# Kernel tuning notes

Measured on AMD Instinct MI355X. Metric: run time of the kernel, lower is better.

The kernel has to match this reference:

```python
import jax, jax.numpy as jnp
import numpy as np

X = 32; Y = 32
H1 = (X + Y) * 10 * 8          # 5120
H2 = X * Y * 4                 # 4096
HID = 1 * (X * X + Y * Y)      # gru_scale_s=1 -> 2048
IN1 = 2 * X + Y + X * Y        # 1120
IN2 = 2 * Y + Y + X * Y        # 1120
OUT1 = X * X; OUT2 = Y * Y


def gru_cell(x, h, Wih, Whh, bih, bhh):
    # PyTorch GRU cell, gate order r,z,n
    gi = Wih @ x + bih
    gh = Whh @ h + bhh
    ir, iz, inn = jnp.split(gi, 3)
    hr, hz, hn = jnp.split(gh, 3)
    r = jax.nn.sigmoid(ir + hr)
    z = jax.nn.sigmoid(iz + hz)
    n = jnp.tanh(inn + r * hn)
    return (1.0 - z) * n + z * h


def setup_inputs() -> dict:
    key = jax.random.key(0)
    ks = iter(jax.random.split(key, 40))
    f32 = jnp.float32
    def rn(shape, scale=0.02):
        return (jax.random.normal(next(ks), shape, dtype=f32) * scale)
    inp = {
        'state_inno': rn((X, 1), 1.0),
        'observation_inno': rn((Y, 1), 1.0),
        'diff_state': rn((X, 1), 1.0),
        'diff_obs': rn((Y, 1), 1.0),
        'linearization_error': rn((Y, 1), 1.0),
        'Jacobian': rn((X * Y, 1), 1.0),
        'l1_W': rn((H1, IN1)), 'l1_b': rn((H1,)),
        'gru1_Wih': rn((3 * HID, H1)), 'gru1_Whh': rn((3 * HID, HID)),
        'gru1_bih': rn((3 * HID,)), 'gru1_bhh': rn((3 * HID,)),
        'l2_W1': rn((H2, HID)), 'l2_b1': rn((H2,)),
        'l2_W2': rn((OUT1, H2)), 'l2_b2': rn((OUT1,)),
        'l3_W': rn((H1, IN2)), 'l3_b': rn((H1,)),
        'gru2_Wih': rn((3 * HID, H1)), 'gru2_Whh': rn((3 * HID, HID)),
        'gru2_bih': rn((3 * HID,)), 'gru2_bhh': rn((3 * HID,)),
        'l4_W1': rn((H2, HID)), 'l4_b1': rn((H2,)),
        'l4_W2': rn((OUT2, H2)), 'l4_b2': rn((OUT2,)),
        'hn1': rn((HID,), 1.0),
        'hn2': rn((HID,), 1.0),
    }
    return inp


def reference(state_inno, observation_inno, diff_state, diff_obs,
              linearization_error, Jacobian,
              l1_W, l1_b, gru1_Wih, gru1_Whh, gru1_bih, gru1_bhh,
              l2_W1, l2_b1, l2_W2, l2_b2,
              l3_W, l3_b, gru2_Wih, gru2_Whh, gru2_bih, gru2_bhh,
              l4_W1, l4_b1, l4_W2, l4_b2, hn1, hn2):
    input1 = jnp.concatenate([state_inno, diff_state, linearization_error, Jacobian], axis=0).reshape(-1)
    input2 = jnp.concatenate([observation_inno, diff_obs, linearization_error, Jacobian], axis=0).reshape(-1)

    l1_out = jax.nn.relu(l1_W @ input1 + l1_b)           # [H1]
    h1 = gru_cell(l1_out, hn1, gru1_Wih, gru1_Whh, gru1_bih, gru1_bhh)  # [HID]
    l2_out = l2_W2 @ jax.nn.relu(l2_W1 @ h1 + l2_b1) + l2_b2
    Pk = l2_out.reshape(X, X)

    l3_out = jax.nn.relu(l3_W @ input2 + l3_b)
    h2 = gru_cell(l3_out, hn2, gru2_Wih, gru2_Whh, gru2_bih, gru2_bhh)
    l4_out = l4_W2 @ jax.nn.relu(l4_W1 @ h2 + l4_b1) + l4_b2
    Sk = l4_out.reshape(Y, Y)
    return (Pk, Sk)
```

## Files before the change

### kernel.cpp

```cpp
#include <hip/hip_runtime.h>
#include <hip/hip_bf16.h>

typedef __attribute__((ext_vector_type(4))) float f32x4;

#define TPB 256

#define IN1F   0
#define IN2F   1120
#define HN1F   2240
#define HN2F   4288
#define L1OUT  6336
#define L3OUT  11456
#define GH1    16576
#define GH2    22720
#define GI1    28864
#define GI2    35008
#define H1OFF  41152
#define H2OFF  43200
#define T1OFF  45248
#define T2OFF  49344


__device__ __forceinline__ void burst2(const float* a,
                                       f32x4& w0, f32x4& w1)
{
    asm volatile(
        "global_load_dwordx4 %0, %2, off\n\t"
        "global_load_dwordx4 %1, %2, off offset:1024\n\t"
        "s_waitcnt vmcnt(0)"
        : "=&v"(w0), "=&v"(w1)
        : "v"(a) : "memory");
}

__device__ __forceinline__ void burst4(const float* a,
                                       f32x4& w0, f32x4& w1, f32x4& w2, f32x4& w3)
{
    asm volatile(
        "global_load_dwordx4 %0, %4, off\n\t"
        "global_load_dwordx4 %1, %4, off offset:1024\n\t"
        "global_load_dwordx4 %2, %4, off offset:2048\n\t"
        "global_load_dwordx4 %3, %4, off offset:3072\n\t"
        "s_waitcnt vmcnt(0)"
        : "=&v"(w0), "=&v"(w1), "=&v"(w2), "=&v"(w3)
        : "v"(a) : "memory");
}

__device__ __forceinline__ void burst5_nt(const float* a, const float* a4,
                                          f32x4& w0, f32x4& w1, f32x4& w2,
                                          f32x4& w3, f32x4& w4)
{
    asm volatile(
        "global_load_dwordx4 %0, %5, off nt\n\t"
        "global_load_dwordx4 %1, %5, off offset:1024 nt\n\t"
        "global_load_dwordx4 %2, %5, off offset:2048 nt\n\t"
        "global_load_dwordx4 %3, %5, off offset:3072 nt\n\t"
        "global_load_dwordx4 %4, %6, off nt\n\t"
        "s_waitcnt vmcnt(0)"
        : "=&v"(w0), "=&v"(w1), "=&v"(w2), "=&v"(w3), "=&v"(w4)
        : "v"(a), "v"(a4) : "memory");
}

__device__ __forceinline__ float dot4(const f32x4& w, const f32x4& x) {
    return w[0]*x[0] + w[1]*x[1] + w[2]*x[2] + w[3]*x[3];
}

__device__ __forceinline__ float wave_reduce(float acc) {
#pragma unroll
    for (int off = 32; off; off >>= 1) acc += __shfl_xor(acc, off, 64);
    return acc;
}

__device__ __forceinline__ void stage_x(const float* __restrict__ x, float* xl, int K)
{
    for (int i = threadIdx.x; i < (K >> 2); i += TPB)
        ((f32x4*)xl)[i] = ((const f32x4*)x)[i];
    __syncthreads();
}


template <int ROWS>
__device__ __forceinline__ void mv5120(
    const float* __restrict__ W, const float* __restrict__ bias,
    float* xl, float* red, int row0, float* __restrict__ y, int act)
{
    const int wid  = threadIdx.x >> 6;
    const int lane = threadIdx.x & 63;
    const int c0   = lane * 4;
    const float* xw = xl + wid * 1280 + c0;

#pragma unroll
    for (int r = 0; r < ROWS; ++r) {
        const float* seg = W + (size_t)(row0 + r) * 5120 + wid * 1280 + c0;
        f32x4 w0, w1, w2, w3, w4;
        burst5_nt(seg, seg + 1024, w0, w1, w2, w3, w4);
        float acc = dot4(w0, *reinterpret_cast<const f32x4*>(xw))
                  + dot4(w1, *reinterpret_cast<const f32x4*>(xw + 256))
                  + dot4(w2, *reinterpret_cast<const f32x4*>(xw + 512))
                  + dot4(w3, *reinterpret_cast<const f32x4*>(xw + 768))
                  + dot4(w4, *reinterpret_cast<const f32x4*>(xw + 1024));
        acc = wave_reduce(acc);
        if (lane == 0) red[r * 4 + wid] = acc;
        __syncthreads();
    }
    if (threadIdx.x < ROWS) {
        int t = threadIdx.x;
        float v = red[t*4] + red[t*4+1] + red[t*4+2] + red[t*4+3] + bias[row0 + t];
        if (act) v = fmaxf(v, 0.f);
        y[row0 + t] = v;
    }
}

template <int ROWS>
__device__ __forceinline__ void mv2048(
    const float* __restrict__ W, const float* __restrict__ bias,
    float* xl, float* red, int row0, float* __restrict__ y, int act)
{
    const int wid  = threadIdx.x >> 6;
    const int lane = threadIdx.x & 63;
    const int c0   = lane * 4;
    const float* xw = xl + wid * 512 + c0;

#pragma unroll
    for (int r = 0; r < ROWS; ++r) {
        const float* seg = W + (size_t)(row0 + r) * 2048 + wid * 512 + c0;
        f32x4 w0, w1;
        burst2(seg, w0, w1);
        float acc = dot4(w0, *reinterpret_cast<const f32x4*>(xw))
                  + dot4(w1, *reinterpret_cast<const f32x4*>(xw + 256));
        acc = wave_reduce(acc);
        if (lane == 0) red[r * 4 + wid] = acc;
        __syncthreads();
    }
    if (threadIdx.x < ROWS) {
        int t = threadIdx.x;
        float v = red[t*4] + red[t*4+1] + red[t*4+2] + red[t*4+3] + bias[row0 + t];
        if (act) v = fmaxf(v, 0.f);
        y[row0 + t] = v;
    }
}

template <int ROWS>
__device__ __forceinline__ void mv4096(
    const float* __restrict__ W, const float* __restrict__ bias,
    float* xl, float* red, int row0, float* __restrict__ y, int act)
{
    const int wid  = threadIdx.x >> 6;
    const int lane = threadIdx.x & 63;
    const int c0   = lane * 4;
    const float* xw = xl + wid * 1024 + c0;

#pragma unroll
    for (int r = 0; r < ROWS; ++r) {
        const float* seg = W + (size_t)(row0 + r) * 4096 + wid * 1024 + c0;
        f32x4 w0, w1, w2, w3;
        burst4(seg, w0, w1, w2, w3);
        float acc = dot4(w0, *reinterpret_cast<const f32x4*>(xw))
                  + dot4(w1, *reinterpret_cast<const f32x4*>(xw + 256))
                  + dot4(w2, *reinterpret_cast<const f32x4*>(xw + 512))
                  + dot4(w3, *reinterpret_cast<const f32x4*>(xw + 768));
        acc = wave_reduce(acc);
        if (lane == 0) red[r * 4 + wid] = acc;
        __syncthreads();
    }
    if (threadIdx.x < ROWS) {
        int t = threadIdx.x;
        float v = red[t*4] + red[t*4+1] + red[t*4+2] + red[t*4+3] + bias[row0 + t];
        if (act) v = fmaxf(v, 0.f);
        y[row0 + t] = v;
    }
}

__device__ __forceinline__ void mv1120(
    const float* __restrict__ W, const float* __restrict__ bias,
    float* xl, int row0, float* __restrict__ y, int act)
{
    const int wid  = threadIdx.x >> 6;
    const int lane = threadIdx.x & 63;
    const int c0   = lane * 4;

#pragma unroll
    for (int step = 0; step < 2; ++step) {
        const int rr = row0 + step * 4 + wid;
        const float* Wr = W + (size_t)rr * 1120;
        f32x4 w0, w1, w2, w3;
        burst4(Wr + c0, w0, w1, w2, w3);
        float acc = dot4(w0, *reinterpret_cast<const f32x4*>(xl + c0))
                  + dot4(w1, *reinterpret_cast<const f32x4*>(xl + 256 + c0))
                  + dot4(w2, *reinterpret_cast<const f32x4*>(xl + 512 + c0))
                  + dot4(w3, *reinterpret_cast<const f32x4*>(xl + 768 + c0));
        if (c0 < 96) {
            const f32x4 wt = *reinterpret_cast<const f32x4*>(Wr + 1024 + c0);
            const f32x4 xt = *reinterpret_cast<const f32x4*>(xl + 1024 + c0);
            acc += dot4(wt, xt);
        }
        acc = wave_reduce(acc);
        if (lane == 0) {
            float v = acc + bias[rr];
            if (act) v = fmaxf(v, 0.f);
            y[rr] = v;
        }
    }
}

__global__ void k_prep(const float* __restrict__ state_inno,
                       const float* __restrict__ obs_inno,
                       const float* __restrict__ diff_state,
                       const float* __restrict__ diff_obs,
                       const float* __restrict__ lin_err,
                       const float* __restrict__ jac,
                       const float* __restrict__ hn1,
                       const float* __restrict__ hn2,
                       float* __restrict__ ws)
{
    int i = blockIdx.x * blockDim.x + threadIdx.x;
    if (i < 1120) {
        float v;
        if (i < 32)       v = state_inno[i];
        else if (i < 64)  v = diff_state[i - 32];
        else if (i < 96)  v = lin_err[i - 64];
        else              v = jac[i - 96];
        ws[IN1F + i] = v;
        float v2;
        if (i < 32)       v2 = obs_inno[i];
        else if (i < 64)  v2 = diff_obs[i - 32];
        else              v2 = v;
        ws[IN2F + i] = v2;
    }
    if (i < 2048) {
        ws[HN1F + i] = hn1[i];
        ws[HN2F + i] = hn2[i];
    }
}

__global__ void __launch_bounds__(TPB)
k_stageA(const float* l1_W, const float* l1_b,
         const float* l3_W, const float* l3_b,
         const float* Whh1, const float* bhh1,
         const float* Whh2, const float* bhh2,
         float* ws)
{
    __shared__ float xl[2048];
    __shared__ float red[8 * 4];
    int bid = blockIdx.x;
    if (bid < 640) {
        stage_x(ws + IN1F, xl, 1120);
        mv1120(l1_W, l1_b, xl, bid * 8, ws + L1OUT, 1);
    } else if (bid < 1280) {
        stage_x(ws + IN2F, xl, 1120);
        mv1120(l3_W, l3_b, xl, (bid - 640) * 8, ws + L3OUT, 1);
    } else if (bid < 2048) {
        stage_x(ws + HN1F, xl, 2048);
        mv2048<8>(Whh1, bhh1, xl, red, (bid - 1280) * 8, ws + GH1, 0);
    } else {
        stage_x(ws + HN2F, xl, 2048);
        mv2048<8>(Whh2, bhh2, xl, red, (bid - 2048) * 8, ws + GH2, 0);
    }
}

__global__ void __launch_bounds__(TPB)
k_stageB(const float* Wih1, const float* bih1,
         const float* Wih2, const float* bih2,
         float* ws)
{
    __shared__ float xl[5120];
    __shared__ float red[6 * 4];
    int bid = blockIdx.x;
    if (bid < 1024) {
        stage_x(ws + L1OUT, xl, 5120);
        mv5120<6>(Wih1, bih1, xl, red, bid * 6, ws + GI1, 0);
    } else {
        stage_x(ws + L3OUT, xl, 5120);
        mv5120<6>(Wih2, bih2, xl, red, (bid - 1024) * 6, ws + GI2, 0);
    }
}

__global__ void k_gru(const float* __restrict__ hn1,
                      const float* __restrict__ hn2,
                      float* __restrict__ ws)
{
    int i = blockIdx.x * blockDim.x + threadIdx.x;
    int b = i >> 11, j = i & 2047;
    const float* gi = ws + (b ? GI2 : GI1);
    const float* gh = ws + (b ? GH2 : GH1);
    const float* hn = b ? hn2 : hn1;
    float r = 1.f / (1.f + expf(-(gi[j] + gh[j])));
    float z = 1.f / (1.f + expf(-(gi[2048 + j] + gh[2048 + j])));
    float n = tanhf(gi[4096 + j] + r * gh[4096 + j]);
    float h = (1.f - z) * n + z * hn[j];
    ws[(b ? H2OFF : H1OFF) + j] = h;
}

__global__ void __launch_bounds__(TPB)
k_stageD(const float* W21, const float* b21,
         const float* W41, const float* b41,
         float* ws)
{
    __shared__ float xl[2048];
    __shared__ float red[8 * 4];
    int bid = blockIdx.x;
    if (bid < 512) {
        stage_x(ws + H1OFF, xl, 2048);
        mv2048<8>(W21, b21, xl, red, bid * 8, ws + T1OFF, 1);
    } else {
        stage_x(ws + H2OFF, xl, 2048);
        mv2048<8>(W41, b41, xl, red, (bid - 512) * 8, ws + T2OFF, 1);
    }
}

__global__ void __launch_bounds__(TPB)
k_stageE(const float* __restrict__ W22, const float* __restrict__ b22,
         const float* __restrict__ W42, const float* __restrict__ b42,
         const float* __restrict__ ws, float* __restrict__ out)
{
    __shared__ float xl[4096];
    __shared__ float red[2 * 4];
    int bid = blockIdx.x;
    if (bid < 512) {
        stage_x(ws + T1OFF, xl, 4096);
        mv4096<2>(W22, b22, xl, red, bid * 2, out, 0);
    } else {
        stage_x(ws + T2OFF, xl, 4096);
        mv4096<2>(W42, b42, xl, red, (bid - 512) * 2, out + 1024, 0);
    }
}

extern "C" void kernel_launch(void* const* d_in, const int* in_sizes, int n_in,
                              void* d_out, int out_size, void* d_ws, size_t ws_size,
                              hipStream_t stream)
{
    const float* state_inno = (const float*)d_in[0];
    const float* obs_inno   = (const float*)d_in[1];
    const float* diff_state = (const float*)d_in[2];
    const float* diff_obs   = (const float*)d_in[3];
    const float* lin_err    = (const float*)d_in[4];
    const float* jac        = (const float*)d_in[5];
    const float* l1_W  = (const float*)d_in[6];
    const float* l1_b  = (const float*)d_in[7];
    const float* g1Wih = (const float*)d_in[8];
    const float* g1Whh = (const float*)d_in[9];
    const float* g1bih = (const float*)d_in[10];
    const float* g1bhh = (const float*)d_in[11];
    const float* l2_W1 = (const float*)d_in[12];
    const float* l2_b1 = (const float*)d_in[13];
    const float* l2_W2 = (const float*)d_in[14];
    const float* l2_b2 = (const float*)d_in[15];
    const float* l3_W  = (const float*)d_in[16];
    const float* l3_b  = (const float*)d_in[17];
    const float* g2Wih = (const float*)d_in[18];
    const float* g2Whh = (const float*)d_in[19];
    const float* g2bih = (const float*)d_in[20];
    const float* g2bhh = (const float*)d_in[21];
    const float* l4_W1 = (const float*)d_in[22];
    const float* l4_b1 = (const float*)d_in[23];
    const float* l4_W2 = (const float*)d_in[24];
    const float* l4_b2 = (const float*)d_in[25];
    const float* hn1   = (const float*)d_in[26];
    const float* hn2   = (const float*)d_in[27];

    float* ws = (float*)d_ws;
    float* out = (float*)d_out;

    hipLaunchKernelGGL(k_prep, dim3(8), dim3(TPB), 0, stream,
                       state_inno, obs_inno, diff_state, diff_obs, lin_err, jac,
                       hn1, hn2, ws);

    hipLaunchKernelGGL(k_stageA, dim3(2816), dim3(TPB), 0, stream,
                       l1_W, l1_b, l3_W, l3_b, g1Whh, g1bhh, g2Whh, g2bhh, ws);

    hipLaunchKernelGGL(k_stageB, dim3(2048), dim3(TPB), 0, stream,
                       g1Wih, g1bih, g2Wih, g2bih, ws);

    hipLaunchKernelGGL(k_gru, dim3(16), dim3(TPB), 0, stream, hn1, hn2, ws);

    hipLaunchKernelGGL(k_stageD, dim3(1024), dim3(TPB), 0, stream,
                       l2_W1, l2_b1, l4_W1, l4_b1, ws);

    hipLaunchKernelGGL(k_stageE, dim3(1024), dim3(TPB), 0, stream,
                       l2_W2, l2_b2, l4_W2, l4_b2, ws, out);
}
```

Baseline: 96.72 us.

## Split Wih matvec into per-wave column chunks reduced with atomics

Replaces the row-blocked 5120-wide input-gate matvec with a flat decomposition. Each wave takes one 256-column chunk of one row per iteration and atomically adds its partial dot product into a GI buffer that k_prep now zeroes. The input bias is moved into the GRU kernel, and the hn copy into the workspace is dropped so stage A reads hn directly. This removes the per-row __syncthreads and the block-level reductions. In exchange it adds many global atomics, uses twice the LDS per block, and keeps fewer loads in flight per wave.

```diff
diff --git a/kernel.cpp b/kernel.cpp
--- a/kernel.cpp
+++ b/kernel.cpp
@@ -45,21 +45,6 @@
         : "v"(a) : "memory");
 }
 
-__device__ __forceinline__ void burst5_nt(const float* a, const float* a4,
-                                          f32x4& w0, f32x4& w1, f32x4& w2,
-                                          f32x4& w3, f32x4& w4)
-{
-    asm volatile(
-        "global_load_dwordx4 %0, %5, off nt\n\t"
-        "global_load_dwordx4 %1, %5, off offset:1024 nt\n\t"
-        "global_load_dwordx4 %2, %5, off offset:2048 nt\n\t"
-        "global_load_dwordx4 %3, %5, off offset:3072 nt\n\t"
-        "global_load_dwordx4 %4, %6, off nt\n\t"
-        "s_waitcnt vmcnt(0)"
-        : "=&v"(w0), "=&v"(w1), "=&v"(w2), "=&v"(w3), "=&v"(w4)
-        : "v"(a), "v"(a4) : "memory");
-}
-
 __device__ __forceinline__ float dot4(const f32x4& w, const f32x4& x) {
     return w[0]*x[0] + w[1]*x[1] + w[2]*x[2] + w[3]*x[3];
 }
@@ -77,38 +62,6 @@
     __syncthreads();
 }
 
-
-template <int ROWS>
-__device__ __forceinline__ void mv5120(
-    const float* __restrict__ W, const float* __restrict__ bias,
-    float* xl, float* red, int row0, float* __restrict__ y, int act)
-{
-    const int wid  = threadIdx.x >> 6;
-    const int lane = threadIdx.x & 63;
-    const int c0   = lane * 4;
-    const float* xw = xl + wid * 1280 + c0;
-
-#pragma unroll
-    for (int r = 0; r < ROWS; ++r) {
-        const float* seg = W + (size_t)(row0 + r) * 5120 + wid * 1280 + c0;
-        f32x4 w0, w1, w2, w3, w4;
-        burst5_nt(seg, seg + 1024, w0, w1, w2, w3, w4);
-        float acc = dot4(w0, *reinterpret_cast<const f32x4*>(xw))
-                  + dot4(w1, *reinterpret_cast<const f32x4*>(xw + 256))
-                  + dot4(w2, *reinterpret_cast<const f32x4*>(xw + 512))
-                  + dot4(w3, *reinterpret_cast<const f32x4*>(xw + 768))
-                  + dot4(w4, *reinterpret_cast<const f32x4*>(xw + 1024));
-        acc = wave_reduce(acc);
-        if (lane == 0) red[r * 4 + wid] = acc;
-        __syncthreads();
-    }
-    if (threadIdx.x < ROWS) {
-        int t = threadIdx.x;
-        float v = red[t*4] + red[t*4+1] + red[t*4+2] + red[t*4+3] + bias[row0 + t];
-        if (act) v = fmaxf(v, 0.f);
-        y[row0 + t] = v;
-    }
-}
 
 template <int ROWS>
 __device__ __forceinline__ void mv2048(
@@ -208,8 +161,6 @@
                        const float* __restrict__ diff_obs,
                        const float* __restrict__ lin_err,
                        const float* __restrict__ jac,
-                       const float* __restrict__ hn1,
-                       const float* __restrict__ hn2,
                        float* __restrict__ ws)
 {
     int i = blockIdx.x * blockDim.x + threadIdx.x;
@@ -226,10 +177,7 @@
         else              v2 = v;
         ws[IN2F + i] = v2;
     }
-    if (i < 2048) {
-        ws[HN1F + i] = hn1[i];
-        ws[HN2F + i] = hn2[i];
-    }
+    ws[GI1 + i] = 0.f;
 }
 
 __global__ void __launch_bounds__(TPB)
@@ -237,6 +185,7 @@
          const float* l3_W, const float* l3_b,
          const float* Whh1, const float* bhh1,
          const float* Whh2, const float* bhh2,
+         const float* hn1, const float* hn2,
          float* ws)
 {
     __shared__ float xl[2048];
@@ -249,43 +198,63 @@
         stage_x(ws + IN2F, xl, 1120);
         mv1120(l3_W, l3_b, xl, (bid - 640) * 8, ws + L3OUT, 1);
     } else if (bid < 2048) {
-        stage_x(ws + HN1F, xl, 2048);
+        stage_x(hn1, xl, 2048);
         mv2048<8>(Whh1, bhh1, xl, red, (bid - 1280) * 8, ws + GH1, 0);
     } else {
-        stage_x(ws + HN2F, xl, 2048);
+        stage_x(hn2, xl, 2048);
         mv2048<8>(Whh2, bhh2, xl, red, (bid - 2048) * 8, ws + GH2, 0);
     }
 }
 
 __global__ void __launch_bounds__(TPB)
-k_stageB(const float* Wih1, const float* bih1,
-         const float* Wih2, const float* bih2,
-         float* ws)
-{
-    __shared__ float xl[5120];
-    __shared__ float red[6 * 4];
-    int bid = blockIdx.x;
-    if (bid < 1024) {
-        stage_x(ws + L1OUT, xl, 5120);
-        mv5120<6>(Wih1, bih1, xl, red, bid * 6, ws + GI1, 0);
-    } else {
-        stage_x(ws + L3OUT, xl, 5120);
-        mv5120<6>(Wih2, bih2, xl, red, (bid - 1024) * 6, ws + GI2, 0);
+k_partB(const float* __restrict__ Wih1, const float* __restrict__ Wih2,
+        float* __restrict__ ws)
+{
+    __shared__ float xl[2 * 5120];
+    for (int i = threadIdx.x; i < 1280; i += TPB)
+        ((f32x4*)xl)[i] = ((const f32x4*)(ws + L1OUT))[i];
+    for (int i = threadIdx.x; i < 1280; i += TPB)
+        ((f32x4*)(xl + 5120))[i] = ((const f32x4*)(ws + L3OUT))[i];
+    __syncthreads();
+
+    const int wid  = threadIdx.x >> 6;
+    const int lane = threadIdx.x & 63;
+    const int g    = blockIdx.x * 4 + wid;
+    const int c4   = lane * 4;
+
+#pragma unroll 2
+    for (int t = 0; t < 30; ++t) {
+        const int c  = t * 8192 + g;
+        const int m  = (c >= 122880) ? 1 : 0;
+        const int cl = c - m * 122880;
+        const int row = cl / 20;
+        const int pos = cl - row * 20;
+        const float* Wb = m ? Wih2 : Wih1;
+        const f32x4 w = __builtin_nontemporal_load(
+            reinterpret_cast<const f32x4*>(Wb + (size_t)row * 5120 + pos * 256 + c4));
+        const f32x4 xv = *reinterpret_cast<const f32x4*>(xl + m * 5120 + pos * 256 + c4);
+        float acc = dot4(w, xv);
+        acc = wave_reduce(acc);
+        if (lane == 0)
+            atomicAdd(ws + (m ? GI2 : GI1) + row, acc);
     }
 }
 
 __global__ void k_gru(const float* __restrict__ hn1,
                       const float* __restrict__ hn2,
+                      const float* __restrict__ bih1,
+                      const float* __restrict__ bih2,
                       float* __restrict__ ws)
 {
     int i = blockIdx.x * blockDim.x + threadIdx.x;
     int b = i >> 11, j = i & 2047;
     const float* gi = ws + (b ? GI2 : GI1);
     const float* gh = ws + (b ? GH2 : GH1);
+    const float* bi = b ? bih2 : bih1;
     const float* hn = b ? hn2 : hn1;
-    float r = 1.f / (1.f + expf(-(gi[j] + gh[j])));
-    float z = 1.f / (1.f + expf(-(gi[2048 + j] + gh[2048 + j])));
-    float n = tanhf(gi[4096 + j] + r * gh[4096 + j]);
+    float r = 1.f / (1.f + expf(-(gi[j] + bi[j] + gh[j])));
+    float z = 1.f / (1.f + expf(-(gi[2048 + j] + bi[2048 + j] + gh[2048 + j])));
+    float n = tanhf(gi[4096 + j] + bi[4096 + j] + r * gh[4096 + j]);
     float h = (1.f - z) * n + z * hn[j];
     ws[(b ? H2OFF : H1OFF) + j] = h;
 }
@@ -360,17 +329,18 @@
     float* ws = (float*)d_ws;
     float* out = (float*)d_out;
 
-    hipLaunchKernelGGL(k_prep, dim3(8), dim3(TPB), 0, stream,
-                       state_inno, obs_inno, diff_state, diff_obs, lin_err, jac,
+    hipLaunchKernelGGL(k_prep, dim3(48), dim3(TPB), 0, stream,
+                       state_inno, obs_inno, diff_state, diff_obs, lin_err, jac, ws);
+
+    hipLaunchKernelGGL(k_stageA, dim3(2816), dim3(TPB), 0, stream,
+                       l1_W, l1_b, l3_W, l3_b, g1Whh, g1bhh, g2Whh, g2bhh,
                        hn1, hn2, ws);
 
-    hipLaunchKernelGGL(k_stageA, dim3(2816), dim3(TPB), 0, stream,
-                       l1_W, l1_b, l3_W, l3_b, g1Whh, g1bhh, g2Whh, g2bhh, ws);
-
-    hipLaunchKernelGGL(k_stageB, dim3(2048), dim3(TPB), 0, stream,
-                       g1Wih, g1bih, g2Wih, g2bih, ws);
-
-    hipLaunchKernelGGL(k_gru, dim3(16), dim3(TPB), 0, stream, hn1, hn2, ws);
+    hipLaunchKernelGGL(k_partB, dim3(2048), dim3(TPB), 0, stream,
+                       g1Wih, g2Wih, ws);
+
+    hipLaunchKernelGGL(k_gru, dim3(16), dim3(TPB), 0, stream,
+                       hn1, hn2, g1bih, g2bih, ws);
 
     hipLaunchKernelGGL(k_stageD, dim3(1024), dim3(TPB), 0, stream,
                        l2_W1, l2_b1, l4_W1, l4_b1, ws);
```

Measured after the change: 128.0 us. 1.32x slower.

## Move Whh matvecs into the Wih gate kernel and drop hidden-state staging

Applied to the files above, without the earlier changes.

Moves the recurrent Whh·h matvecs out of the first stage and into the Wih gate kernel, interleaving blocks 4:3 so the large Wih streams and the Whh streams share one launch. The l1/l3 kernel becomes smaller and reads only 1120-element inputs, and the prep kernel no longer copies hn1/hn2 into the workspace because stage_x reads them directly. The aim is to balance bandwidth-bound work across stages and shorten the critical path. The gate kernel now always reserves 5120 floats of shared memory, which may reduce occupancy for the Whh blocks.

```diff
diff --git a/kernel.cpp b/kernel.cpp
--- a/kernel.cpp
+++ b/kernel.cpp
@@ -7,8 +7,6 @@
 
 #define IN1F   0
 #define IN2F   1120
-#define HN1F   2240
-#define HN2F   4288
 #define L1OUT  6336
 #define L3OUT  11456
 #define GH1    16576
@@ -208,8 +206,6 @@
                        const float* __restrict__ diff_obs,
                        const float* __restrict__ lin_err,
                        const float* __restrict__ jac,
-                       const float* __restrict__ hn1,
-                       const float* __restrict__ hn2,
                        float* __restrict__ ws)
 {
     int i = blockIdx.x * blockDim.x + threadIdx.x;
@@ -226,51 +222,54 @@
         else              v2 = v;
         ws[IN2F + i] = v2;
     }
-    if (i < 2048) {
-        ws[HN1F + i] = hn1[i];
-        ws[HN2F + i] = hn2[i];
-    }
 }
 
 __global__ void __launch_bounds__(TPB)
-k_stageA(const float* l1_W, const float* l1_b,
-         const float* l3_W, const float* l3_b,
-         const float* Whh1, const float* bhh1,
-         const float* Whh2, const float* bhh2,
-         float* ws)
-{
-    __shared__ float xl[2048];
-    __shared__ float red[8 * 4];
+k_l1l3(const float* l1_W, const float* l1_b,
+       const float* l3_W, const float* l3_b,
+       float* ws)
+{
+    __shared__ float xl[1120];
     int bid = blockIdx.x;
     if (bid < 640) {
         stage_x(ws + IN1F, xl, 1120);
         mv1120(l1_W, l1_b, xl, bid * 8, ws + L1OUT, 1);
-    } else if (bid < 1280) {
+    } else {
         stage_x(ws + IN2F, xl, 1120);
         mv1120(l3_W, l3_b, xl, (bid - 640) * 8, ws + L3OUT, 1);
-    } else if (bid < 2048) {
-        stage_x(ws + HN1F, xl, 2048);
-        mv2048<8>(Whh1, bhh1, xl, red, (bid - 1280) * 8, ws + GH1, 0);
+    }
+}
+
+__global__ void __launch_bounds__(TPB)
+k_gates(const float* Wih1, const float* bih1,
+        const float* Wih2, const float* bih2,
+        const float* Whh1, const float* bhh1,
+        const float* Whh2, const float* bhh2,
+        const float* hn1, const float* hn2,
+        float* ws)
+{
+    __shared__ float xl[5120];
+    __shared__ float red[8 * 4];
+    const int g = blockIdx.x / 7;
+    const int r = blockIdx.x % 7;
+    if (r < 4) {
+        int w = g * 4 + r;
+        if (w < 1024) {
+            stage_x(ws + L1OUT, xl, 5120);
+            mv5120<6>(Wih1, bih1, xl, red, w * 6, ws + GI1, 0);
+        } else {
+            stage_x(ws + L3OUT, xl, 5120);
+            mv5120<6>(Wih2, bih2, xl, red, (w - 1024) * 6, ws + GI2, 0);
+        }
     } else {
-        stage_x(ws + HN2F, xl, 2048);
-        mv2048<8>(Whh2, bhh2, xl, red, (bid - 2048) * 8, ws + GH2, 0);
-    }
-}
-
-__global__ void __launch_bounds__(TPB)
-k_stageB(const float* Wih1, const float* bih1,
-         const float* Wih2, const float* bih2,
-         float* ws)
-{
-    __shared__ float xl[5120];
-    __shared__ float red[6 * 4];
-    int bid = blockIdx.x;
-    if (bid < 1024) {
-        stage_x(ws + L1OUT, xl, 5120);
-        mv5120<6>(Wih1, bih1, xl, red, bid * 6, ws + GI1, 0);
-    } else {
-        stage_x(ws + L3OUT, xl, 5120);
-        mv5120<6>(Wih2, bih2, xl, red, (bid - 1024) * 6, ws + GI2, 0);
+        int w = g * 3 + (r - 4);
+        if (w < 768) {
+            stage_x(hn1, xl, 2048);
+            mv2048<8>(Whh1, bhh1, xl, red, w * 8, ws + GH1, 0);
+        } else {
+            stage_x(hn2, xl, 2048);
+            mv2048<8>(Whh2, bhh2, xl, red, (w - 768) * 8, ws + GH2, 0);
+        }
     }
 }
 
@@ -360,15 +359,15 @@
     float* ws = (float*)d_ws;
     float* out = (float*)d_out;
 
-    hipLaunchKernelGGL(k_prep, dim3(8), dim3(TPB), 0, stream,
-                       state_inno, obs_inno, diff_state, diff_obs, lin_err, jac,
-                       hn1, hn2, ws);
-
-    hipLaunchKernelGGL(k_stageA, dim3(2816), dim3(TPB), 0, stream,
-                       l1_W, l1_b, l3_W, l3_b, g1Whh, g1bhh, g2Whh, g2bhh, ws);
-
-    hipLaunchKernelGGL(k_stageB, dim3(2048), dim3(TPB), 0, stream,
-                       g1Wih, g1bih, g2Wih, g2bih, ws);
+    hipLaunchKernelGGL(k_prep, dim3(5), dim3(TPB), 0, stream,
+                       state_inno, obs_inno, diff_state, diff_obs, lin_err, jac, ws);
+
+    hipLaunchKernelGGL(k_l1l3, dim3(1280), dim3(TPB), 0, stream,
+                       l1_W, l1_b, l3_W, l3_b, ws);
+
+    hipLaunchKernelGGL(k_gates, dim3(3584), dim3(TPB), 0, stream,
+                       g1Wih, g1bih, g2Wih, g2bih,
+                       g1Whh, g1bhh, g2Whh, g2bhh, hn1, hn2, ws);
 
     hipLaunchKernelGGL(k_gru, dim3(16), dim3(TPB), 0, stream, hn1, hn2, ws);
 
```

Result: faster. 93.79 us (-3.0%).
